# Optimization experiments

Measured on AMD Instinct MI355X. Metric: run time of the kernel, lower is better.

The kernel has to match this reference:

```python
import jax, jax.numpy as jnp
import numpy as np

B, H, W, C = 8, 64, 64, 512
D = C // 8  # key/query/value projection dim per SAGAN block


def setup_inputs() -> dict:
    key = jax.random.key(0)
    ks = jax.random.split(key, 5)
    scale = 1.0 / np.sqrt(C)
    return {
        "x": jax.random.normal(ks[0], (B, H, W, C), dtype=jnp.float32),
        "Wf": jax.random.normal(ks[1], (C, D), dtype=jnp.float32) * scale,
        "bf": jnp.zeros((D,), dtype=jnp.float32),
        "Wg": jax.random.normal(ks[2], (C, D), dtype=jnp.float32) * scale,
        "bg": jnp.zeros((D,), dtype=jnp.float32),
        "Wh": jax.random.normal(ks[3], (C, D), dtype=jnp.float32) * scale,
        "bh": jnp.zeros((D,), dtype=jnp.float32),
        "Wv": jax.random.normal(ks[4], (D, C), dtype=jnp.float32) * (1.0 / np.sqrt(D)),
        "bv": jnp.zeros((C,), dtype=jnp.float32),
        "gamma": jnp.float32(0.01),
    }


def reference(x, Wf, bf, Wg, bg, Wh, bh, Wv, bv, gamma):
    b, h, w, c = x.shape
    n = h * w
    xf = x.reshape(b, n, c)  # flatten spatial dims: [B, N, C]
    # 1x1 convs == per-position dense projections
    f = xf @ Wf + bf  # [B, N, D]
    g = xf @ Wg + bg  # [B, N, D]
    hh = xf @ Wh + bh  # [B, N, D]
    # unscaled attention logits, softmax over keys (axis=-1)
    s = jnp.einsum("bnd,bmd->bnm", f, g)  # [B, N, N]
    attn = jax.nn.softmax(s, axis=-1)
    context = jnp.einsum("bnm,bmd->bnd", attn, hh)  # [B, N, D]
    # v conv (1x1) applied to gamma-scaled context, residual add
    o = (gamma * context) @ Wv + bv + xf  # [B, N, C]
    return o.reshape(b, h, w, c)
```

## Files before the change

### kernel.cpp

```cpp
#include <hip/hip_runtime.h>
#include <hip/hip_bf16.h>
#include <math.h>


typedef short v8s __attribute__((ext_vector_type(8)));
typedef unsigned short v4u __attribute__((ext_vector_type(4)));
typedef unsigned v4i __attribute__((ext_vector_type(4)));
typedef float v4f __attribute__((ext_vector_type(4)));

#define BB 8
#define NN 4096
#define CC 512
#define DD 64

__device__ __forceinline__ unsigned short f2bf(float f){
  union { float f; unsigned u; } v; v.f = f;
  unsigned r = (v.u + 0x7FFF + ((v.u >> 16) & 1)) >> 16;
  return (unsigned short)r;
}

#if __has_builtin(__builtin_amdgcn_cvt_pk_bf16_f32)
typedef __bf16 bf2_t __attribute__((ext_vector_type(2)));
__device__ __forceinline__ unsigned pkbf(float a, float b){
  bf2_t r = __builtin_amdgcn_cvt_pk_bf16_f32(a, b);
  union { bf2_t v; unsigned u; } c; c.v = r; return c.u;
}
#else
__device__ __forceinline__ unsigned pkbf(float a, float b){
  return (unsigned)f2bf(a) | ((unsigned)f2bf(b) << 16);
}
#endif

__device__ __forceinline__ void gload_lds16(const void* g, void* l){
  __builtin_amdgcn_global_load_lds(
      (const __attribute__((address_space(1))) void*)g,
      (__attribute__((address_space(3))) void*)l, 16, 0, 0);
}

__global__ void transpose_w(const float* __restrict__ Wf,
                            const float* __restrict__ Wg,
                            const float* __restrict__ Wh,
                            const float* __restrict__ Wv,
                            unsigned short* __restrict__ Wt,
                            unsigned short* __restrict__ Wvt){
  int idx = blockIdx.x * 256 + threadIdx.x;
  if (idx < 3 * DD * CC){
    int p = idx / (DD * CC); int rem = idx % (DD * CC);
    int d = rem / CC; int c = rem % CC;
    const float* W = (p == 0) ? Wf : ((p == 1) ? Wg : Wh);
    Wt[idx] = f2bf(W[c * DD + d]);
  } else {
    int idx2 = idx - 3 * DD * CC;
    if (idx2 < CC * DD){
      int c = idx2 / DD; int d = idx2 % DD;
      Wvt[idx2] = f2bf(Wv[d * CC + c]);
    }
  }
}

__global__ __launch_bounds__(256) void proj_kernel(
    const float* __restrict__ x,
    const unsigned short* __restrict__ Wt,
    const float* __restrict__ bf_,
    const float* __restrict__ bg_,
    const float* __restrict__ bh_,
    unsigned short* __restrict__ f,
    unsigned short* __restrict__ g,
    unsigned short* __restrict__ ht)
{
  __shared__ __align__(16) short lA[64][72];
  __shared__ __align__(16) short lB[192][72];
  int t = threadIdx.x;
  int w = t >> 6, lane = t & 63;
  int quad = lane >> 4, l16 = lane & 15;
  int rowbase = blockIdx.x * 64;
  int m0 = w * 16;

  v4f acc[12];
  #pragma unroll
  for (int i = 0; i < 12; i++) acc[i] = (v4f){0.f, 0.f, 0.f, 0.f};

  int arow = t >> 2, aq4 = t & 3;
  for (int kt = 0; kt < 8; ++kt){
    int k0 = kt * 64;
    {
      const float* xp = x + (rowbase + arow) * 512 + k0 + aq4 * 16;
      v4f a0 = *(const v4f*)(xp);
      v4f a1 = *(const v4f*)(xp + 4);
      v4f a2 = *(const v4f*)(xp + 8);
      v4f a3 = *(const v4f*)(xp + 12);
      v4i c0 = { pkbf(a0[0],a0[1]), pkbf(a0[2],a0[3]),
                 pkbf(a1[0],a1[1]), pkbf(a1[2],a1[3]) };
      v4i c1 = { pkbf(a2[0],a2[1]), pkbf(a2[2],a2[3]),
                 pkbf(a3[0],a3[1]), pkbf(a3[2],a3[3]) };
      *(v4i*)&lA[arow][aq4 * 16]     = c0;
      *(v4i*)&lA[arow][aq4 * 16 + 8] = c1;
    }
    #pragma unroll
    for (int r = 0; r < 6; r++){
      int chunk = t + r * 256;
      int row = chunk >> 3, c8 = chunk & 7;
      *(v8s*)&lB[row][c8 * 8] = *(const v8s*)(Wt + row * 512 + k0 + c8 * 8);
    }
    __syncthreads();
    v8s A0 = *(const v8s*)&lA[m0 + l16][quad * 8];
    v8s A1 = *(const v8s*)&lA[m0 + l16][quad * 8 + 32];
    #pragma unroll
    for (int cb = 0; cb < 12; ++cb){
      v8s b0 = *(const v8s*)&lB[cb * 16 + l16][quad * 8];
      v8s b1 = *(const v8s*)&lB[cb * 16 + l16][quad * 8 + 32];
      acc[cb] = __builtin_amdgcn_mfma_f32_16x16x32_bf16(A0, b0, acc[cb], 0, 0, 0);
      acc[cb] = __builtin_amdgcn_mfma_f32_16x16x32_bf16(A1, b1, acc[cb], 0, 0, 0);
    }
    __syncthreads();
  }

  #pragma unroll
  for (int cb = 0; cb < 8; ++cb){
    int col = cb * 16 + l16;
    int p = col >> 6, d = col & 63;
    float bb = (p == 0) ? bf_[d] : bg_[d];
    #pragma unroll
    for (int r = 0; r < 4; r++){
      int gr = rowbase + m0 + quad * 4 + r;
      float val = acc[cb][r] + bb;
      if (p == 0) f[gr * 64 + d] = f2bf(val * 1.44269504f);
      else        g[gr * 64 + d] = f2bf(val);
    }
  }

  short (*lT)[65] = (short(*)[65])lB;
  #pragma unroll
  for (int cb = 8; cb < 12; ++cb){
    int d = (cb - 8) * 16 + l16;
    float bb = bh_[d];
    #pragma unroll
    for (int r = 0; r < 4; r++)
      lT[m0 + quad * 4 + r][d] = (short)f2bf(acc[cb][r] + bb);
  }
  __syncthreads();
  {
    int dd = t >> 2, nb = t & 3;
    v8s h0, h1;
    #pragma unroll
    for (int i = 0; i < 8; i++){
      h0[i] = lT[nb * 16 + i][dd];
      h1[i] = lT[nb * 16 + 8 + i][dd];
    }
    int bidx = rowbase >> 12;
    int n0 = (rowbase & 4095) + nb * 16;
    unsigned short* hp = ht + ((size_t)(bidx * 64 + dd)) * 4096 + n0;
    *(v8s*)hp = h0;
    *(v8s*)(hp + 8) = h1;
  }
}

__global__ __launch_bounds__(256) void flash_kernel(
    const unsigned short* __restrict__ f,
    const unsigned short* __restrict__ g,
    const unsigned short* __restrict__ ht,
    float* __restrict__ Opart,
    float* __restrict__ lipart,
    unsigned short* __restrict__ ctx,
    int niter, int direct)
{
  __shared__ __align__(16) short lK[64 * 64];
  __shared__ __align__(16) short lV[64 * 64];
  __shared__ __align__(16) short lP[4][16][72];
  int t = threadIdx.x;
  int w = t >> 6, lane = t & 63;
  int quad = lane >> 4, l16 = lane & 15;
  int qt = blockIdx.x, sp = blockIdx.y, b = blockIdx.z;
  int q0 = qt * 64;
  int m0 = w * 16;

  const unsigned short* fb = f  + b * NN * 64;
  const unsigned short* gb = g  + b * NN * 64;
  const unsigned short* hb = ht + b * 64 * NN;

  v8s QB0 = *(const v8s*)(fb + (q0 + m0 + l16) * 64 + quad * 8);
  v8s QB1 = *(const v8s*)(fb + (q0 + m0 + l16) * 64 + quad * 8 + 32);

  int j0 = sp * niter;
  const char* srcK[2]; const char* srcV[2];
  char* dstK[2]; char* dstV[2];
  #pragma unroll
  for (int k = 0; k < 2; k++){
    int row = w * 16 + k * 8 + (lane >> 3);
    int c = (lane & 7) ^ (row & 7);
    srcK[k] = (const char*)gb + (size_t)j0 * 8192 + row * 128 + c * 16;
    srcV[k] = (const char*)hb + (size_t)row * 8192 + (size_t)j0 * 128 + c * 16;
    dstK[k] = (char*)lK + w * 2048 + k * 1024;
    dstV[k] = (char*)lV + w * 2048 + k * 1024;
  }

  int ph = quad ^ (l16 & 7);
  const short* kA0 = lK + l16 * 64 + ph * 8;
  const short* kA1 = lK + l16 * 64 + (ph ^ 4) * 8;
  const short* vB0 = lV + l16 * 64 + ph * 8;
  const short* vB1 = lV + l16 * 64 + (ph ^ 4) * 8;

  float rsum = 0.f;
  v4f O[4];
  #pragma unroll
  for (int cb = 0; cb < 4; cb++) O[cb] = (v4f){0.f, 0.f, 0.f, 0.f};

  for (int jj = 0; jj < niter; ++jj){
    #pragma unroll
    for (int k = 0; k < 2; k++){
      gload_lds16(srcK[k], dstK[k]);
      gload_lds16(srcV[k], dstV[k]);
      srcK[k] += 8192; srcV[k] += 128;
    }
    __syncthreads();

    v4f st[4];
    #pragma unroll
    for (int cb = 0; cb < 4; cb++){
      v8s a0 = *(const v8s*)(kA0 + cb * 1024);
      v8s a1 = *(const v8s*)(kA1 + cb * 1024);
      v4f z = (v4f){0.f, 0.f, 0.f, 0.f};
      z = __builtin_amdgcn_mfma_f32_16x16x32_bf16(a0, QB0, z, 0, 0, 0);
      st[cb] = __builtin_amdgcn_mfma_f32_16x16x32_bf16(a1, QB1, z, 0, 0, 0);
    }

    #pragma unroll
    for (int cb = 0; cb < 4; cb++){
      float p0 = exp2f(st[cb][0]);
      float p1 = exp2f(st[cb][1]);
      float p2 = exp2f(st[cb][2]);
      float p3 = exp2f(st[cb][3]);
      rsum += (p0 + p1) + (p2 + p3);
      unsigned d0 = __builtin_amdgcn_perm(__float_as_uint(p1), __float_as_uint(p0), 0x07060302u);
      unsigned d1 = __builtin_amdgcn_perm(__float_as_uint(p3), __float_as_uint(p2), 0x07060302u);
      uint2 pk; pk.x = d0; pk.y = d1;
      *(uint2*)&lP[w][l16][cb * 16 + quad * 4] = pk;
    }

    v8s PA0 = *(const v8s*)&lP[w][l16][quad * 8];
    v8s PA1 = *(const v8s*)&lP[w][l16][quad * 8 + 32];
    #pragma unroll
    for (int cb = 0; cb < 4; cb++){
      v8s vb0 = *(const v8s*)(vB0 + cb * 1024);
      v8s vb1 = *(const v8s*)(vB1 + cb * 1024);
      O[cb] = __builtin_amdgcn_mfma_f32_16x16x32_bf16(PA0, vb0, O[cb], 0, 0, 0);
      O[cb] = __builtin_amdgcn_mfma_f32_16x16x32_bf16(PA1, vb1, O[cb], 0, 0, 0);
    }
    __syncthreads();
  }

  rsum += __shfl_xor(rsum, 16, 64);
  rsum += __shfl_xor(rsum, 32, 64);

  if (direct){
    float inv[4];
    #pragma unroll
    for (int r = 0; r < 4; r++)
      inv[r] = 1.0f / __shfl(rsum, quad * 4 + r, 64);
    #pragma unroll
    for (int cb = 0; cb < 4; cb++)
      #pragma unroll
      for (int r = 0; r < 4; r++){
        int row = q0 + m0 + quad * 4 + r;
        ctx[(b * NN + row) * 64 + cb * 16 + l16] = f2bf(O[cb][r] * inv[r]);
      }
  } else {
    int bf = (b * 64 + qt) * 4 + sp;
    if (quad == 0) lipart[bf * 64 + m0 + l16] = rsum;
    float* Ob = Opart + (size_t)bf * 4096;
    #pragma unroll
    for (int cb = 0; cb < 4; cb++)
      #pragma unroll
      for (int r = 0; r < 4; r++)
        Ob[(m0 + quad * 4 + r) * 64 + cb * 16 + l16] = O[cb][r];
  }
}

__global__ __launch_bounds__(256) void reduce_kernel(
    const float* __restrict__ Opart,
    const float* __restrict__ lipart,
    unsigned short* __restrict__ ctx)
{
  int i4 = blockIdx.x * 256 + threadIdx.x;
  int bqt = i4 >> 10;
  int rem = (i4 & 1023) << 2;
  int rl  = rem >> 6;
  const float* Ob  = Opart  + (size_t)bqt * 4 * 4096;
  const float* lib = lipart + bqt * 4 * 64;
  v4f s = *(const v4f*)(Ob + rem);
  s = s + *(const v4f*)(Ob + 4096  + rem);
  s = s + *(const v4f*)(Ob + 8192  + rem);
  s = s + *(const v4f*)(Ob + 12288 + rem);
  float li = (lib[rl] + lib[64 + rl]) + (lib[128 + rl] + lib[192 + rl]);
  float inv = 1.0f / li;
  uint2 o; o.x = pkbf(s[0] * inv, s[1] * inv); o.y = pkbf(s[2] * inv, s[3] * inv);
  *(uint2*)(ctx + (size_t)bqt * 4096 + rem) = o;
}

__global__ __launch_bounds__(256) void outproj_kernel(
    const unsigned short* __restrict__ ctx,
    const unsigned short* __restrict__ Wvt,
    const float* __restrict__ bv,
    const float* __restrict__ x,
    const float* __restrict__ gamma_p,
    float* __restrict__ out)
{
  __shared__ __align__(16) short lA[64][72];
  __shared__ __align__(16) short lB[128][72];
  int t = threadIdx.x;
  int w = t >> 6, lane = t & 63;
  int quad = lane >> 4, l16 = lane & 15;
  int rowbase = blockIdx.x * 64;
  int colbase = blockIdx.y * 128;
  float gamma = *gamma_p;

  #pragma unroll
  for (int r = 0; r < 2; r++){
    int chunk = t + r * 256;
    int row = chunk >> 3, c8 = chunk & 7;
    *(v8s*)&lA[row][c8 * 8] = *(const v8s*)(ctx + (rowbase + row) * 64 + c8 * 8);
  }
  #pragma unroll
  for (int r = 0; r < 4; r++){
    int chunk = t + r * 256;
    int row = chunk >> 3, c8 = chunk & 7;
    *(v8s*)&lB[row][c8 * 8] = *(const v8s*)(Wvt + (colbase + row) * 64 + c8 * 8);
  }
  __syncthreads();
  int m0 = w * 16;
  v8s A0 = *(const v8s*)&lA[m0 + l16][quad * 8];
  v8s A1 = *(const v8s*)&lA[m0 + l16][quad * 8 + 32];
  v4f acc[8];
  #pragma unroll
  for (int cb = 0; cb < 8; cb++){
    v8s b0 = *(const v8s*)&lB[cb * 16 + l16][quad * 8];
    v8s b1 = *(const v8s*)&lB[cb * 16 + l16][quad * 8 + 32];
    v4f z = (v4f){0.f, 0.f, 0.f, 0.f};
    z = __builtin_amdgcn_mfma_f32_16x16x32_bf16(A0, b0, z, 0, 0, 0);
    acc[cb] = __builtin_amdgcn_mfma_f32_16x16x32_bf16(A1, b1, z, 0, 0, 0);
  }
  #pragma unroll
  for (int cb = 0; cb < 8; cb++){
    int col = colbase + cb * 16 + l16;
    float bvv = bv[col];
    #pragma unroll
    for (int r = 0; r < 4; r++){
      int gr = rowbase + m0 + quad * 4 + r;
      out[gr * 512 + col] = gamma * acc[cb][r] + bvv + x[gr * 512 + col];
    }
  }
}

extern "C" void kernel_launch(void* const* d_in, const int* in_sizes, int n_in,
                              void* d_out, int out_size, void* d_ws, size_t ws_size,
                              hipStream_t stream) {
  const float* x   = (const float*)d_in[0];
  const float* Wf  = (const float*)d_in[1];
  const float* bf_ = (const float*)d_in[2];
  const float* Wg  = (const float*)d_in[3];
  const float* bg  = (const float*)d_in[4];
  const float* Wh  = (const float*)d_in[5];
  const float* bh  = (const float*)d_in[6];
  const float* Wv  = (const float*)d_in[7];
  const float* bv  = (const float*)d_in[8];
  const float* gam = (const float*)d_in[9];
  float* out = (float*)d_out;

  char* ws = (char*)d_ws;
  unsigned short* Wt  = (unsigned short*)(ws);
  unsigned short* Wvt = (unsigned short*)(ws + 196608);
  unsigned short* f   = (unsigned short*)(ws + 262144);
  unsigned short* g   = (unsigned short*)(ws + 4456448);
  unsigned short* ht  = (unsigned short*)(ws + 8650752);
  unsigned short* ctx = (unsigned short*)(ws + 12845056);
  float* Opart  = (float*)(ws + 17039360);
  float* lipart = (float*)(ws + 50593792);

  transpose_w<<<512, 256, 0, stream>>>(Wf, Wg, Wh, Wv, Wt, Wvt);
  proj_kernel<<<512, 256, 0, stream>>>(x, Wt, bf_, bg, bh, f, g, ht);

  bool split = (ws_size >= (size_t)51118080);
  if (split){
    flash_kernel<<<dim3(64, 4, 8), 256, 0, stream>>>(f, g, ht, Opart, lipart, ctx, 16, 0);
    reduce_kernel<<<2048, 256, 0, stream>>>(Opart, lipart, ctx);
  } else {
    flash_kernel<<<dim3(64, 1, 8), 256, 0, stream>>>(f, g, ht, nullptr, nullptr, ctx, 64, 1);
  }
  outproj_kernel<<<dim3(512, 4), 256, 0, stream>>>(ctx, Wvt, bv, x, gam, out);
}
```

Measured before the change: 227.9 us.

## Double-buffer K/V tiles, compute row sums via MFMA, use native exp2

Splits the K and V shared-memory tiles into two buffers so the next tile's global-to-LDS loads are issued before computing on the current tile, overlapping memory latency with MFMA work. The per-row softmax denominator is now accumulated by an extra MFMA against a vector of bf16 ones, replacing scalar adds and cross-lane shuffles. exp2f is swapped for the hardware exp2 intrinsic. The row sum now uses bf16-rounded probabilities, which matches what is multiplied with V. The loop assumes niter is even.

```diff
diff --git a/kernel.cpp b/kernel.cpp
--- a/kernel.cpp
+++ b/kernel.cpp
@@ -29,6 +29,12 @@
 __device__ __forceinline__ unsigned pkbf(float a, float b){
   return (unsigned)f2bf(a) | ((unsigned)f2bf(b) << 16);
 }
+#endif
+
+#if __has_builtin(__builtin_amdgcn_exp2f)
+__device__ __forceinline__ float ex2(float x){ return __builtin_amdgcn_exp2f(x); }
+#else
+__device__ __forceinline__ float ex2(float x){ return exp2f(x); }
 #endif
 
 __device__ __forceinline__ void gload_lds16(const void* g, void* l){
@@ -164,8 +170,8 @@
     unsigned short* __restrict__ ctx,
     int niter, int direct)
 {
-  __shared__ __align__(16) short lK[64 * 64];
-  __shared__ __align__(16) short lV[64 * 64];
+  __shared__ __align__(16) short lK[2][64 * 64];
+  __shared__ __align__(16) short lV[2][64 * 64];
   __shared__ __align__(16) short lP[4][16][72];
   int t = threadIdx.x;
   int w = t >> 6, lane = t & 63;
@@ -183,42 +189,55 @@
 
   int j0 = sp * niter;
   const char* srcK[2]; const char* srcV[2];
-  char* dstK[2]; char* dstV[2];
+  char* dstK[2][2]; char* dstV[2][2];
   #pragma unroll
   for (int k = 0; k < 2; k++){
     int row = w * 16 + k * 8 + (lane >> 3);
     int c = (lane & 7) ^ (row & 7);
     srcK[k] = (const char*)gb + (size_t)j0 * 8192 + row * 128 + c * 16;
     srcV[k] = (const char*)hb + (size_t)row * 8192 + (size_t)j0 * 128 + c * 16;
-    dstK[k] = (char*)lK + w * 2048 + k * 1024;
-    dstV[k] = (char*)lV + w * 2048 + k * 1024;
+    #pragma unroll
+    for (int b2 = 0; b2 < 2; b2++){
+      dstK[b2][k] = (char*)lK[b2] + w * 2048 + k * 1024;
+      dstV[b2][k] = (char*)lV[b2] + w * 2048 + k * 1024;
+    }
   }
 
   int ph = quad ^ (l16 & 7);
-  const short* kA0 = lK + l16 * 64 + ph * 8;
-  const short* kA1 = lK + l16 * 64 + (ph ^ 4) * 8;
-  const short* vB0 = lV + l16 * 64 + ph * 8;
-  const short* vB1 = lV + l16 * 64 + (ph ^ 4) * 8;
-
-  float rsum = 0.f;
+  const short* kA0[2]; const short* kA1[2];
+  const short* vB0[2]; const short* vB1[2];
+  #pragma unroll
+  for (int b2 = 0; b2 < 2; b2++){
+    kA0[b2] = lK[b2] + l16 * 64 + ph * 8;
+    kA1[b2] = lK[b2] + l16 * 64 + (ph ^ 4) * 8;
+    vB0[b2] = lV[b2] + l16 * 64 + ph * 8;
+    vB1[b2] = lV[b2] + l16 * 64 + (ph ^ 4) * 8;
+  }
+
+  v8s ones;
+  #pragma unroll
+  for (int i = 0; i < 8; i++) ones[i] = (short)0x3F80;
+
+  v4f rz = (v4f){0.f, 0.f, 0.f, 0.f};
   v4f O[4];
   #pragma unroll
   for (int cb = 0; cb < 4; cb++) O[cb] = (v4f){0.f, 0.f, 0.f, 0.f};
 
-  for (int jj = 0; jj < niter; ++jj){
+  auto stage = [&](int b2){
     #pragma unroll
     for (int k = 0; k < 2; k++){
-      gload_lds16(srcK[k], dstK[k]);
-      gload_lds16(srcV[k], dstV[k]);
+      gload_lds16(srcK[k], dstK[b2][k]);
+      gload_lds16(srcV[k], dstV[b2][k]);
       srcK[k] += 8192; srcV[k] += 128;
     }
-    __syncthreads();
-
+  };
+
+  auto compute = [&](int b2){
     v4f st[4];
     #pragma unroll
     for (int cb = 0; cb < 4; cb++){
-      v8s a0 = *(const v8s*)(kA0 + cb * 1024);
-      v8s a1 = *(const v8s*)(kA1 + cb * 1024);
+      v8s a0 = *(const v8s*)(kA0[b2] + cb * 1024);
+      v8s a1 = *(const v8s*)(kA1[b2] + cb * 1024);
       v4f z = (v4f){0.f, 0.f, 0.f, 0.f};
       z = __builtin_amdgcn_mfma_f32_16x16x32_bf16(a0, QB0, z, 0, 0, 0);
       st[cb] = __builtin_amdgcn_mfma_f32_16x16x32_bf16(a1, QB1, z, 0, 0, 0);
@@ -226,11 +245,10 @@
 
     #pragma unroll
     for (int cb = 0; cb < 4; cb++){
-      float p0 = exp2f(st[cb][0]);
-      float p1 = exp2f(st[cb][1]);
-      float p2 = exp2f(st[cb][2]);
-      float p3 = exp2f(st[cb][3]);
-      rsum += (p0 + p1) + (p2 + p3);
+      float p0 = ex2(st[cb][0]);
+      float p1 = ex2(st[cb][1]);
+      float p2 = ex2(st[cb][2]);
+      float p3 = ex2(st[cb][3]);
       unsigned d0 = __builtin_amdgcn_perm(__float_as_uint(p1), __float_as_uint(p0), 0x07060302u);
       unsigned d1 = __builtin_amdgcn_perm(__float_as_uint(p3), __float_as_uint(p2), 0x07060302u);
       uint2 pk; pk.x = d0; pk.y = d1;
@@ -239,24 +257,35 @@
 
     v8s PA0 = *(const v8s*)&lP[w][l16][quad * 8];
     v8s PA1 = *(const v8s*)&lP[w][l16][quad * 8 + 32];
+
+    rz = __builtin_amdgcn_mfma_f32_16x16x32_bf16(PA0, ones, rz, 0, 0, 0);
+    rz = __builtin_amdgcn_mfma_f32_16x16x32_bf16(PA1, ones, rz, 0, 0, 0);
+
     #pragma unroll
     for (int cb = 0; cb < 4; cb++){
-      v8s vb0 = *(const v8s*)(vB0 + cb * 1024);
-      v8s vb1 = *(const v8s*)(vB1 + cb * 1024);
+      v8s vb0 = *(const v8s*)(vB0[b2] + cb * 1024);
+      v8s vb1 = *(const v8s*)(vB1[b2] + cb * 1024);
       O[cb] = __builtin_amdgcn_mfma_f32_16x16x32_bf16(PA0, vb0, O[cb], 0, 0, 0);
       O[cb] = __builtin_amdgcn_mfma_f32_16x16x32_bf16(PA1, vb1, O[cb], 0, 0, 0);
     }
+  };
+
+  stage(0);
+  __syncthreads();
+  for (int jj = 0; jj < niter; jj += 2){
+    stage(1);
+    compute(0);
     __syncthreads();
-  }
-
-  rsum += __shfl_xor(rsum, 16, 64);
-  rsum += __shfl_xor(rsum, 32, 64);
+    if (jj + 2 < niter) stage(0);
+    compute(1);
+    __syncthreads();
+  }
 
   if (direct){
     float inv[4];
     #pragma unroll
     for (int r = 0; r < 4; r++)
-      inv[r] = 1.0f / __shfl(rsum, quad * 4 + r, 64);
+      inv[r] = 1.0f / rz[r];
     #pragma unroll
     for (int cb = 0; cb < 4; cb++)
       #pragma unroll
@@ -266,7 +295,11 @@
       }
   } else {
     int bf = (b * 64 + qt) * 4 + sp;
-    if (quad == 0) lipart[bf * 64 + m0 + l16] = rsum;
+    if (l16 == 0){
+      #pragma unroll
+      for (int r = 0; r < 4; r++)
+        lipart[bf * 64 + m0 + quad * 4 + r] = rz[r];
+    }
     float* Ob = Opart + (size_t)bf * 4096;
     #pragma unroll
     for (int cb = 0; cb < 4; cb++)
```

Result: faster. 220.3 us (-3.3%).
